# Kernel optimization log

Hardware: AMD Instinct MI355X
Metric: run time of the kernel (lower is better)

The kernel has to match this reference:

```python
import jax, jax.numpy as jnp
import numpy as np

N = 50000      # nodes
E = 1600000    # edges (avg degree 32)
IN, H, OUT, ED = 16, 128, 64, 16


def setup_inputs() -> dict:
    key = jax.random.key(0)
    ks = jax.random.split(key, 24)

    def w(k, shape):
        return jax.random.normal(k, shape, jnp.float32) / np.float32(np.sqrt(shape[0]))

    inp = {
        "x": jax.random.normal(ks[0], (N, IN), jnp.float32),
        "edge_attr": jax.random.normal(ks[1], (E, ED), jnp.float32),
        "edge_src": jax.random.randint(ks[2], (E,), 0, N, jnp.int32),
        "edge_dst": jax.random.randint(ks[3], (E,), 0, N, jnp.int32),
    }
    dims = [(IN, H, H), (H, H, H), (H, H, OUT)]
    i = 4
    for l, (din, dh, dout) in enumerate(dims):
        inp[f"we{l}"] = w(ks[i], (ED, din)); inp[f"be{l}"] = jnp.zeros((din,), jnp.float32)
        inp[f"w1{l}"] = w(ks[i + 1], (din, dh)); inp[f"b1{l}"] = jnp.zeros((dh,), jnp.float32)
        inp[f"w2{l}"] = w(ks[i + 2], (dh, dout)); inp[f"b2{l}"] = jnp.zeros((dout,), jnp.float32)
        i += 3
    inp["rw1"] = w(ks[i], (OUT, H)); inp["rb1"] = jnp.zeros((H,), jnp.float32)
    inp["rw2"] = w(ks[i + 1], (H, IN)); inp["rb2"] = jnp.zeros((IN,), jnp.float32)
    return inp


def reference(x, edge_attr, edge_src, edge_dst,
              we0, be0, w10, b10, w20, b20,
              we1, be1, w11, b11, w21, b21,
              we2, be2, w12, b12, w22, b22,
              rw1, rb1, rw2, rb2):
    layers = [(we0, be0, w10, b10, w20, b20),
              (we1, be1, w11, b11, w21, b21),
              (we2, be2, w12, b12, w22, b22)]
    n = x.shape[0]

    def phi(h):
        # GIN with edge features (GINE): h_i = MLP(h_i + sum_j relu(h_j + W_e e_ij))
        for idx, (we, be, w1, b1, w2, b2) in enumerate(layers):
            e = edge_attr @ we + be                                  # [E, d_in]
            msg = jax.nn.relu(h[edge_src] + e)                       # [E, d_in]
            agg = jax.ops.segment_sum(msg, edge_dst, num_segments=n)  # [N, d_in]
            h = jax.nn.relu((h + agg) @ w1 + b1) @ w2 + b2           # conv MLP
            if idx < len(layers) - 1:
                h = jax.nn.relu(h)
        return h

    out = phi(x) + phi(-x)                       # sign invariance, [N, OUT]
    out = jax.nn.relu(out @ rw1 + rb1) @ rw2 + rb2  # rho readout, [N, IN]
    return out
```

## Files before the change

### kernel.cpp

```cpp
#include <hip/hip_runtime.h>

constexpr int DHID = 128;

typedef __attribute__((ext_vector_type(8))) short bf16x8v;
typedef __attribute__((ext_vector_type(4))) float f32x4v;

__device__ __forceinline__ float b2f(unsigned short u) {
    union { unsigned int i; float f; } v;
    v.i = ((unsigned int)u) << 16;
    return v.f;
}
__device__ __forceinline__ unsigned short f2b(float f) {
    union { float f; unsigned int i; } v;
    v.f = f;
    unsigned int x = v.i;
    return (unsigned short)((x + 0x7fff + ((x >> 16) & 1)) >> 16);
}
__device__ __forceinline__ unsigned int pack2(float a, float b) {
    return (unsigned int)f2b(a) | ((unsigned int)f2b(b) << 16);
}
__device__ __forceinline__ float bres(float w) { return w - b2f(f2b(w)); }
__device__ __forceinline__ void dot2b(float& acc, unsigned int a, unsigned int b) {
    asm("v_dot2_f32_bf16 %0, %1, %2, %0" : "+v"(acc) : "v"(a), "v"(b));
}

__global__ __launch_bounds__(256)
void init_h0(const float* __restrict__ x, float* __restrict__ H0,
             unsigned short* __restrict__ H0B, int n) {
    int i = blockIdx.x * 256 + threadIdx.x;
    if (i < n * 16) {
        int r = i >> 4, c = i & 15;
        float v = x[i];
        H0[(size_t)(2 * r) * 16 + c] = v;
        H0[(size_t)(2 * r + 1) * 16 + c] = -v;
        H0B[(size_t)(2 * r) * 16 + c] = f2b(v);
        H0B[(size_t)(2 * r + 1) * 16 + c] = f2b(-v);
    }
}

__global__ __launch_bounds__(256)
void sum_signs(const float* __restrict__ H3, float* __restrict__ S, int n) {
    int i = blockIdx.x * 256 + threadIdx.x;
    if (i < n * 64) {
        int r = i >> 6;
        S[i] = H3[i + (size_t)r * 64] + H3[i + (size_t)r * 64 + 64];
    }
}

__global__ __launch_bounds__(256)
void csr_count(const int* __restrict__ DST, int* __restrict__ deg, int E_) {
    int e = blockIdx.x * 256 + threadIdx.x;
    if (e < E_) atomicAdd(&deg[DST[e]], 1);
}

__global__ __launch_bounds__(256)
void scan1(const int* __restrict__ deg, int* __restrict__ off,
           int* __restrict__ bsum, int n) {
    __shared__ int s[256];
    int tid = threadIdx.x;
    int i = blockIdx.x * 256 + tid;
    int v = (i < n) ? deg[i] : 0;
    s[tid] = v;
    __syncthreads();
    for (int d = 1; d < 256; d <<= 1) {
        int t = (tid >= d) ? s[tid - d] : 0;
        __syncthreads();
        if (tid >= d) s[tid] += t;
        __syncthreads();
    }
    if (i < n) off[i] = s[tid] - v;
    if (tid == 255) bsum[blockIdx.x] = s[255];
}

__global__ __launch_bounds__(256)
void scan2(int* __restrict__ bsum, int nb) {
    __shared__ int s[256];
    int tid = threadIdx.x;
    int v = (tid < nb) ? bsum[tid] : 0;
    s[tid] = v;
    __syncthreads();
    for (int d = 1; d < 256; d <<= 1) {
        int t = (tid >= d) ? s[tid - d] : 0;
        __syncthreads();
        if (tid >= d) s[tid] += t;
        __syncthreads();
    }
    if (tid < nb) bsum[tid] = s[tid] - v;
}

__global__ __launch_bounds__(256)
void scan3(int* __restrict__ off, int* __restrict__ pos,
           const int* __restrict__ bsum, const int* __restrict__ deg, int n) {
    int i = blockIdx.x * 256 + threadIdx.x;
    if (i < n) {
        int o = off[i] + bsum[blockIdx.x];
        off[i] = o;
        pos[i] = o;
        if (i == n - 1) off[n] = o + deg[i];
    }
}

__global__ __launch_bounds__(256)
void csr_fill(const int* __restrict__ SRC, const int* __restrict__ DST,
              const float* __restrict__ EA, int* __restrict__ pos,
              int* __restrict__ csrsrc, uint4* __restrict__ EABS, int E_) {
    int e = blockIdx.x * 256 + threadIdx.x;
    if (e < E_) {
        int d = DST[e];
        int j = atomicAdd(&pos[d], 1);
        csrsrc[j] = SRC[e];
        const float4* ea4 = (const float4*)(EA + (size_t)e * 16);
        float4 q0 = ea4[0], q1 = ea4[1], q2 = ea4[2], q3 = ea4[3];
        uint4 o0, o1;
        o0.x = pack2(q0.x, q0.y); o0.y = pack2(q0.z, q0.w);
        o0.z = pack2(q1.x, q1.y); o0.w = pack2(q1.z, q1.w);
        o1.x = pack2(q2.x, q2.y); o1.y = pack2(q2.z, q2.w);
        o1.z = pack2(q3.x, q3.y); o1.w = pack2(q3.z, q3.w);
        EABS[(size_t)2 * j] = o0;
        EABS[(size_t)2 * j + 1] = o1;
    }
}

__global__ __launch_bounds__(256)
void agg_gather128(const int* __restrict__ CSRS, const int* __restrict__ OFF,
                   const unsigned short* __restrict__ EABS,
                   const float* __restrict__ WE, const float* __restrict__ BE,
                   const unsigned short* __restrict__ HB,
                   float* __restrict__ AGG, int n) {
    __shared__ float esm_all[4][16][132];
    const int tid = threadIdx.x;
    const int wv = tid >> 6;
    const int lane = tid & 63;
    const int node = blockIdx.x * 4 + wv;
    if (node >= n) return;
    float (*esm)[132] = esm_all[wv];

    const int col = lane & 15;
    const int grp = lane >> 4;
    const int klo = (grp & 1) * 8;

    bf16x8v bfrag[8];
#pragma unroll
    for (int cb = 0; cb < 8; ++cb) {
        bf16x8v b;
#pragma unroll
        for (int i = 0; i < 8; ++i) {
            float w = WE[(klo + i) * 128 + cb * 16 + col];
            unsigned short hi = f2b(w);
            unsigned short lo = f2b(bres(w));
            b[i] = (short)(grp >= 2 ? lo : hi);
        }
        bfrag[cb] = b;
    }
    float bias[8];
#pragma unroll
    for (int cb = 0; cb < 8; ++cb) bias[cb] = BE[cb * 16 + col];

    const int o = lane & 31;
    const int s = o >> 4;
    const int co = (o & 15) * 8;
    const int ep = lane >> 5;

    float acc[8];
#pragma unroll
    for (int i = 0; i < 8; ++i) acc[i] = 0.f;

    const int j0 = OFF[node], j1 = OFF[node + 1];
    const char* ebase = (const char*)EABS;

    for (int base = j0; base < j1; base += 16) {
        const int rem = j1 - base;
        uint4 a4 = *(const uint4*)(ebase + ((size_t)(base + col) << 5) +
                                   ((grp & 1) << 4));
        bf16x8v afrag = __builtin_bit_cast(bf16x8v, a4);
#pragma unroll
        for (int cb = 0; cb < 8; ++cb) {
            f32x4v c = {bias[cb], bias[cb], bias[cb], bias[cb]};
            f32x4v ev = __builtin_amdgcn_mfma_f32_16x16x32_bf16(afrag, bfrag[cb],
                                                                c, 0, 0, 0);
#pragma unroll
            for (int r = 0; r < 4; ++r) {
                const int slot = grp * 4 + r;
                esm[slot][cb * 16 + col] = (slot < rem) ? ev[r] : -1e30f;
            }
        }
#pragma unroll
        for (int i = 0; i < 8; ++i) {
            const int er = 2 * i + ep;
            const int eidx = base + er;
            const int src = CSRS[eidx < j1 ? eidx : (j1 - 1)];
            uint4 hv = *(const uint4*)(HB + (((size_t)(2 * src + s)) << 7) + co);
            const float4* ep4 = (const float4*)&esm[er][co];
            float4 e0 = ep4[0], e1 = ep4[1];
            acc[0] += fmaxf(b2f(hv.x & 0xffff) + e0.x, 0.f);
            acc[1] += fmaxf(b2f(hv.x >> 16)    + e0.y, 0.f);
            acc[2] += fmaxf(b2f(hv.y & 0xffff) + e0.z, 0.f);
            acc[3] += fmaxf(b2f(hv.y >> 16)    + e0.w, 0.f);
            acc[4] += fmaxf(b2f(hv.z & 0xffff) + e1.x, 0.f);
            acc[5] += fmaxf(b2f(hv.z >> 16)    + e1.y, 0.f);
            acc[6] += fmaxf(b2f(hv.w & 0xffff) + e1.z, 0.f);
            acc[7] += fmaxf(b2f(hv.w >> 16)    + e1.w, 0.f);
        }
    }
#pragma unroll
    for (int i = 0; i < 8; ++i) acc[i] += __shfl_xor(acc[i], 32);
    if (lane < 32) {
        float* arow = AGG + (size_t)(2 * node + s) * 128 + co;
        float4 v0 = make_float4(acc[0], acc[1], acc[2], acc[3]);
        float4 v1 = make_float4(acc[4], acc[5], acc[6], acc[7]);
        ((float4*)arow)[0] = v0;
        ((float4*)arow)[1] = v1;
    }
}

__global__ __launch_bounds__(256)
void agg_gather16(const int* __restrict__ CSRS, const int* __restrict__ OFF,
                  const uint4* __restrict__ EABS, const float* __restrict__ WE,
                  const float* __restrict__ BE,
                  const unsigned short* __restrict__ HB,
                  float* __restrict__ AGG, int n) {
    const int l = threadIdx.x & 31;
    const int node = blockIdx.x * 8 + (threadIdx.x >> 5);
    if (node >= n) return;
    const int s = l >> 4;
    const int c = l & 15;
    unsigned int wh[8], wl[8];
#pragma unroll
    for (int t = 0; t < 8; ++t) {
        float a0 = WE[(2 * t) * 16 + c], a1 = WE[(2 * t + 1) * 16 + c];
        wh[t] = pack2(a0, a1);
        wl[t] = pack2(bres(a0), bres(a1));
    }
    const float bev = BE[c];
    float acc = 0.f;
    const int j0 = OFF[node], j1 = OFF[node + 1];
#pragma unroll 4
    for (int j = j0; j < j1; ++j) {
        int src = CSRS[j];
        uint4 p = EABS[(size_t)2 * j], q = EABS[(size_t)2 * j + 1];
        float ec = bev;
        dot2b(ec, p.x, wh[0]); dot2b(ec, p.y, wh[1]);
        dot2b(ec, p.z, wh[2]); dot2b(ec, p.w, wh[3]);
        dot2b(ec, q.x, wh[4]); dot2b(ec, q.y, wh[5]);
        dot2b(ec, q.z, wh[6]); dot2b(ec, q.w, wh[7]);
        dot2b(ec, p.x, wl[0]); dot2b(ec, p.y, wl[1]);
        dot2b(ec, p.z, wl[2]); dot2b(ec, p.w, wl[3]);
        dot2b(ec, q.x, wl[4]); dot2b(ec, q.y, wl[5]);
        dot2b(ec, q.z, wl[6]); dot2b(ec, q.w, wl[7]);
        float hv = b2f(HB[(size_t)(2 * src + s) * 16 + c]);
        acc += fmaxf(hv + ec, 0.f);
    }
    AGG[(size_t)(2 * node + s) * 16 + c] = acc;
}

template <int DIN, int DOUT, bool RELU_OUT, bool HAS_AGG, bool WRITE_B>
__global__ __launch_bounds__(256)
void node_mlp(const float* __restrict__ X, const float* __restrict__ AGG,
              const float* __restrict__ W1, const float* __restrict__ B1,
              const float* __restrict__ W2, const float* __restrict__ B2,
              float* __restrict__ OUT, unsigned short* __restrict__ OUTB,
              int rows) {
    __shared__ float sX[32 * DIN];
    __shared__ float sH[32 * DHID];
    const int tid = threadIdx.x;

    for (int row0 = blockIdx.x * 32; row0 < rows; row0 += gridDim.x * 32) {
        __syncthreads();
        constexpr int DIN4 = DIN / 4;
        for (int i = tid; i < 32 * DIN4; i += 256) {
            int r = i / DIN4, k4 = i % DIN4;
            int gr = row0 + r;
            float4 v = make_float4(0.f, 0.f, 0.f, 0.f);
            if (gr < rows) {
                v = ((const float4*)X)[(size_t)gr * DIN4 + k4];
                if (HAS_AGG) {
                    float4 a = ((const float4*)AGG)[(size_t)gr * DIN4 + k4];
                    v.x += a.x; v.y += a.y; v.z += a.z; v.w += a.w;
                }
            }
            ((float4*)sX)[i] = v;
        }
        __syncthreads();
        {
            const int c = tid & 63;
            const int r0 = tid >> 6;
            float acc[8][2];
            const float b1a = B1[c], b1b = B1[c + 64];
#pragma unroll
            for (int j = 0; j < 8; ++j) {
                acc[j][0] = b1a;
                acc[j][1] = b1b;
            }
#pragma unroll 2
            for (int k4 = 0; k4 < DIN / 4; ++k4) {
                const int k = 4 * k4;
                float wa[4], wb[4];
#pragma unroll
                for (int kk = 0; kk < 4; ++kk) {
                    wa[kk] = W1[(k + kk) * DHID + c];
                    wb[kk] = W1[(k + kk) * DHID + c + 64];
                }
#pragma unroll
                for (int j = 0; j < 8; ++j) {
                    float4 xv = ((const float4*)sX)[((r0 + 4 * j) * DIN + k) >> 2];
                    acc[j][0] += xv.x * wa[0]; acc[j][1] += xv.x * wb[0];
                    acc[j][0] += xv.y * wa[1]; acc[j][1] += xv.y * wb[1];
                    acc[j][0] += xv.z * wa[2]; acc[j][1] += xv.z * wb[2];
                    acc[j][0] += xv.w * wa[3]; acc[j][1] += xv.w * wb[3];
                }
            }
#pragma unroll
            for (int j = 0; j < 8; ++j) {
                int r = r0 + 4 * j;
                sH[r * DHID + c] = fmaxf(acc[j][0], 0.f);
                sH[r * DHID + c + 64] = fmaxf(acc[j][1], 0.f);
            }
        }
        __syncthreads();
        {
            constexpr int HALF = DOUT / 2;
            constexpr int RP = 256 / HALF;
            constexpr int ITER = 32 / RP;
            const int c = tid % HALF;
            const int r0 = tid / HALF;
            float acc[ITER][2];
            const float bz0 = B2[c], bz1 = B2[c + HALF];
#pragma unroll
            for (int j = 0; j < ITER; ++j) {
                acc[j][0] = bz0;
                acc[j][1] = bz1;
            }
#pragma unroll 2
            for (int k4 = 0; k4 < DHID / 4; ++k4) {
                const int k = 4 * k4;
                float wa[4], wb[4];
#pragma unroll
                for (int kk = 0; kk < 4; ++kk) {
                    wa[kk] = W2[(k + kk) * DOUT + c];
                    wb[kk] = W2[(k + kk) * DOUT + c + HALF];
                }
#pragma unroll
                for (int j = 0; j < ITER; ++j) {
                    float4 hv = ((const float4*)sH)[((r0 + RP * j) * DHID + k) >> 2];
                    acc[j][0] += hv.x * wa[0]; acc[j][1] += hv.x * wb[0];
                    acc[j][0] += hv.y * wa[1]; acc[j][1] += hv.y * wb[1];
                    acc[j][0] += hv.z * wa[2]; acc[j][1] += hv.z * wb[2];
                    acc[j][0] += hv.w * wa[3]; acc[j][1] += hv.w * wb[3];
                }
            }
#pragma unroll
            for (int j = 0; j < ITER; ++j) {
                int gr = row0 + r0 + RP * j;
                if (gr < rows) {
                    float o0 = acc[j][0], o1 = acc[j][1];
                    if (RELU_OUT) {
                        o0 = fmaxf(o0, 0.f);
                        o1 = fmaxf(o1, 0.f);
                    }
                    OUT[(size_t)gr * DOUT + c] = o0;
                    OUT[(size_t)gr * DOUT + c + HALF] = o1;
                    if (WRITE_B) {
                        OUTB[(size_t)gr * DOUT + c] = f2b(o0);
                        OUTB[(size_t)gr * DOUT + c + HALF] = f2b(o1);
                    }
                }
            }
        }
    }
}

extern "C" void kernel_launch(void* const* d_in, const int* in_sizes, int n_in,
                              void* d_out, int out_size, void* d_ws, size_t ws_size,
                              hipStream_t stream) {
    const float* x = (const float*)d_in[0];
    const float* ea = (const float*)d_in[1];
    const int* esrc = (const int*)d_in[2];
    const int* edst = (const int*)d_in[3];
    const float* we0 = (const float*)d_in[4];
    const float* be0 = (const float*)d_in[5];
    const float* w10 = (const float*)d_in[6];
    const float* b10 = (const float*)d_in[7];
    const float* w20 = (const float*)d_in[8];
    const float* b20 = (const float*)d_in[9];
    const float* we1 = (const float*)d_in[10];
    const float* be1 = (const float*)d_in[11];
    const float* w11 = (const float*)d_in[12];
    const float* b11 = (const float*)d_in[13];
    const float* w21 = (const float*)d_in[14];
    const float* b21 = (const float*)d_in[15];
    const float* we2 = (const float*)d_in[16];
    const float* be2 = (const float*)d_in[17];
    const float* w12 = (const float*)d_in[18];
    const float* b12 = (const float*)d_in[19];
    const float* w22 = (const float*)d_in[20];
    const float* b22 = (const float*)d_in[21];
    const float* rw1 = (const float*)d_in[22];
    const float* rb1 = (const float*)d_in[23];
    const float* rw2 = (const float*)d_in[24];
    const float* rb2 = (const float*)d_in[25];

    const int N = in_sizes[0] / 16;
    const int E = in_sizes[2];
    const int M = 2 * N;

    float* HA = (float*)d_ws;
    float* HB = HA + (size_t)M * 128;
    float* AG = HB + (size_t)M * 128;
    unsigned short* Hb = (unsigned short*)(AG + (size_t)M * 128);
    unsigned short* EABS = Hb + (size_t)M * 128;
    int* deg = (int*)(EABS + (size_t)E * 16);
    int* off = deg + N;
    int* pos = off + N + 1;
    int* bsum = pos + N;
    int* csrsrc = bsum + 256;

    const int ntiles = (M + 31) / 32;
    const int eblocks = (E + 255) / 256;
    const int nblocks = (N + 255) / 256;

    hipMemsetAsync(deg, 0, (size_t)N * sizeof(int), stream);
    csr_count<<<eblocks, 256, 0, stream>>>(edst, deg, E);
    scan1<<<nblocks, 256, 0, stream>>>(deg, off, bsum, N);
    scan2<<<1, 256, 0, stream>>>(bsum, nblocks);
    scan3<<<nblocks, 256, 0, stream>>>(off, pos, bsum, deg, N);
    csr_fill<<<eblocks, 256, 0, stream>>>(esrc, edst, ea, pos, csrsrc,
                                          (uint4*)EABS, E);

    init_h0<<<(N * 16 + 255) / 256, 256, 0, stream>>>(x, HA, Hb, N);

    agg_gather16<<<(N + 7) / 8, 256, 0, stream>>>(csrsrc, off, (const uint4*)EABS,
                                                  we0, be0, Hb, AG, N);
    node_mlp<16, 128, true, true, true><<<ntiles, 256, 0, stream>>>(
        HA, AG, w10, b10, w20, b20, HB, Hb, M);

    agg_gather128<<<(N + 3) / 4, 256, 0, stream>>>(csrsrc, off, EABS,
                                                   we1, be1, Hb, AG, N);
    node_mlp<128, 128, true, true, true><<<ntiles, 256, 0, stream>>>(
        HB, AG, w11, b11, w21, b21, HA, Hb, M);

    agg_gather128<<<(N + 3) / 4, 256, 0, stream>>>(csrsrc, off, EABS,
                                                   we2, be2, Hb, AG, N);
    node_mlp<128, 64, false, true, false><<<ntiles, 256, 0, stream>>>(
        HA, AG, w12, b12, w22, b22, HB, nullptr, M);

    sum_signs<<<(N * 64 + 255) / 256, 256, 0, stream>>>(HB, AG, N);
    node_mlp<64, 16, false, false, false><<<(N + 31) / 32, 256, 0, stream>>>(
        AG, nullptr, rw1, rb1, rw2, rb2, (float*)d_out, nullptr, N);
}
```

Measured before the change: 955.0 us.

## Use persistent grid-stride gather kernels with full-tile fast path and packed adds

The gather kernels become persistent with a fixed grid of 1024 blocks that grid-stride over nodes. The per-wave weight-fragment setup (the WE to bf16 hi/lo split) is therefore amortized across many nodes instead of being redone for each one. The 128-wide gather also splits full 16-edge tiles from the remainder tile, dropping masking and index clamping in the common path, and uses v_pk_add_f32 for the accumulation. A fixed grid of 1024 blocks may leave load imbalance or underfill on a large GPU.

```diff
diff --git a/kernel.cpp b/kernel.cpp
--- a/kernel.cpp
+++ b/kernel.cpp
@@ -4,6 +4,7 @@
 
 typedef __attribute__((ext_vector_type(8))) short bf16x8v;
 typedef __attribute__((ext_vector_type(4))) float f32x4v;
+typedef __attribute__((ext_vector_type(2))) float f32x2v;
 
 __device__ __forceinline__ float b2f(unsigned short u) {
     union { unsigned int i; float f; } v;
@@ -22,6 +23,11 @@
 __device__ __forceinline__ float bres(float w) { return w - b2f(f2b(w)); }
 __device__ __forceinline__ void dot2b(float& acc, unsigned int a, unsigned int b) {
     asm("v_dot2_f32_bf16 %0, %1, %2, %0" : "+v"(acc) : "v"(a), "v"(b));
+}
+__device__ __forceinline__ f32x2v pkadd(f32x2v a, f32x2v b) {
+    f32x2v d;
+    asm("v_pk_add_f32 %0, %1, %2" : "=v"(d) : "v"(a), "v"(b));
+    return d;
 }
 
 __global__ __launch_bounds__(256)
@@ -131,8 +137,6 @@
     const int tid = threadIdx.x;
     const int wv = tid >> 6;
     const int lane = tid & 63;
-    const int node = blockIdx.x * 4 + wv;
-    if (node >= n) return;
     float (*esm)[132] = esm_all[wv];
 
     const int col = lane & 15;
@@ -161,55 +165,106 @@
     const int co = (o & 15) * 8;
     const int ep = lane >> 5;
 
-    float acc[8];
-#pragma unroll
-    for (int i = 0; i < 8; ++i) acc[i] = 0.f;
-
-    const int j0 = OFF[node], j1 = OFF[node + 1];
     const char* ebase = (const char*)EABS;
-
-    for (int base = j0; base < j1; base += 16) {
-        const int rem = j1 - base;
-        uint4 a4 = *(const uint4*)(ebase + ((size_t)(base + col) << 5) +
-                                   ((grp & 1) << 4));
-        bf16x8v afrag = __builtin_bit_cast(bf16x8v, a4);
-#pragma unroll
-        for (int cb = 0; cb < 8; ++cb) {
-            f32x4v c = {bias[cb], bias[cb], bias[cb], bias[cb]};
-            f32x4v ev = __builtin_amdgcn_mfma_f32_16x16x32_bf16(afrag, bfrag[cb],
-                                                                c, 0, 0, 0);
-#pragma unroll
-            for (int r = 0; r < 4; ++r) {
-                const int slot = grp * 4 + r;
-                esm[slot][cb * 16 + col] = (slot < rem) ? ev[r] : -1e30f;
-            }
-        }
-#pragma unroll
-        for (int i = 0; i < 8; ++i) {
-            const int er = 2 * i + ep;
-            const int eidx = base + er;
-            const int src = CSRS[eidx < j1 ? eidx : (j1 - 1)];
-            uint4 hv = *(const uint4*)(HB + (((size_t)(2 * src + s)) << 7) + co);
-            const float4* ep4 = (const float4*)&esm[er][co];
-            float4 e0 = ep4[0], e1 = ep4[1];
-            acc[0] += fmaxf(b2f(hv.x & 0xffff) + e0.x, 0.f);
-            acc[1] += fmaxf(b2f(hv.x >> 16)    + e0.y, 0.f);
-            acc[2] += fmaxf(b2f(hv.y & 0xffff) + e0.z, 0.f);
-            acc[3] += fmaxf(b2f(hv.y >> 16)    + e0.w, 0.f);
-            acc[4] += fmaxf(b2f(hv.z & 0xffff) + e1.x, 0.f);
-            acc[5] += fmaxf(b2f(hv.z >> 16)    + e1.y, 0.f);
-            acc[6] += fmaxf(b2f(hv.w & 0xffff) + e1.z, 0.f);
-            acc[7] += fmaxf(b2f(hv.w >> 16)    + e1.w, 0.f);
-        }
-    }
-#pragma unroll
-    for (int i = 0; i < 8; ++i) acc[i] += __shfl_xor(acc[i], 32);
-    if (lane < 32) {
-        float* arow = AGG + (size_t)(2 * node + s) * 128 + co;
-        float4 v0 = make_float4(acc[0], acc[1], acc[2], acc[3]);
-        float4 v1 = make_float4(acc[4], acc[5], acc[6], acc[7]);
-        ((float4*)arow)[0] = v0;
-        ((float4*)arow)[1] = v1;
+    const int stride = gridDim.x * 4;
+
+    for (int node = blockIdx.x * 4 + wv; node < n; node += stride) {
+        f32x2v acc[4];
+#pragma unroll
+        for (int i = 0; i < 4; ++i) { acc[i].x = 0.f; acc[i].y = 0.f; }
+
+        const int j0 = OFF[node], j1 = OFF[node + 1];
+        int base = j0;
+        for (; base + 16 <= j1; base += 16) {
+            uint4 a4 = *(const uint4*)(ebase + ((size_t)(base + col) << 5) +
+                                       ((grp & 1) << 4));
+            bf16x8v afrag = __builtin_bit_cast(bf16x8v, a4);
+#pragma unroll
+            for (int cb = 0; cb < 8; ++cb) {
+                f32x4v c = {bias[cb], bias[cb], bias[cb], bias[cb]};
+                f32x4v ev = __builtin_amdgcn_mfma_f32_16x16x32_bf16(
+                    afrag, bfrag[cb], c, 0, 0, 0);
+#pragma unroll
+                for (int r = 0; r < 4; ++r)
+                    esm[grp * 4 + r][cb * 16 + col] = ev[r];
+            }
+#pragma unroll
+            for (int i = 0; i < 8; ++i) {
+                const int er = 2 * i + ep;
+                const int src = CSRS[base + er];
+                uint4 hv = *(const uint4*)(HB + (((size_t)(2 * src + s)) << 7) + co);
+                const float4* ep4 = (const float4*)&esm[er][co];
+                float4 e0 = ep4[0], e1 = ep4[1];
+                f32x2v h, e2, t;
+                h.x = b2f(hv.x & 0xffff); h.y = b2f(hv.x >> 16);
+                e2.x = e0.x; e2.y = e0.y;
+                t = pkadd(h, e2);
+                t.x = fmaxf(t.x, 0.f); t.y = fmaxf(t.y, 0.f);
+                acc[0] = pkadd(acc[0], t);
+                h.x = b2f(hv.y & 0xffff); h.y = b2f(hv.y >> 16);
+                e2.x = e0.z; e2.y = e0.w;
+                t = pkadd(h, e2);
+                t.x = fmaxf(t.x, 0.f); t.y = fmaxf(t.y, 0.f);
+                acc[1] = pkadd(acc[1], t);
+                h.x = b2f(hv.z & 0xffff); h.y = b2f(hv.z >> 16);
+                e2.x = e1.x; e2.y = e1.y;
+                t = pkadd(h, e2);
+                t.x = fmaxf(t.x, 0.f); t.y = fmaxf(t.y, 0.f);
+                acc[2] = pkadd(acc[2], t);
+                h.x = b2f(hv.w & 0xffff); h.y = b2f(hv.w >> 16);
+                e2.x = e1.z; e2.y = e1.w;
+                t = pkadd(h, e2);
+                t.x = fmaxf(t.x, 0.f); t.y = fmaxf(t.y, 0.f);
+                acc[3] = pkadd(acc[3], t);
+            }
+        }
+        if (base < j1) {
+            const int rem = j1 - base;
+            uint4 a4 = *(const uint4*)(ebase +
+                                       ((size_t)(base + (col < rem ? col : 0)) << 5) +
+                                       ((grp & 1) << 4));
+            bf16x8v afrag = __builtin_bit_cast(bf16x8v, a4);
+#pragma unroll
+            for (int cb = 0; cb < 8; ++cb) {
+                f32x4v c = {bias[cb], bias[cb], bias[cb], bias[cb]};
+                f32x4v ev = __builtin_amdgcn_mfma_f32_16x16x32_bf16(
+                    afrag, bfrag[cb], c, 0, 0, 0);
+#pragma unroll
+                for (int r = 0; r < 4; ++r) {
+                    const int slot = grp * 4 + r;
+                    esm[slot][cb * 16 + col] = (slot < rem) ? ev[r] : -1e30f;
+                }
+            }
+#pragma unroll
+            for (int i = 0; i < 8; ++i) {
+                const int er = 2 * i + ep;
+                const int eidx = base + er;
+                const int src = CSRS[eidx < j1 ? eidx : (j1 - 1)];
+                uint4 hv = *(const uint4*)(HB + (((size_t)(2 * src + s)) << 7) + co);
+                const float4* ep4 = (const float4*)&esm[er][co];
+                float4 e0 = ep4[0], e1 = ep4[1];
+                acc[0].x += fmaxf(b2f(hv.x & 0xffff) + e0.x, 0.f);
+                acc[0].y += fmaxf(b2f(hv.x >> 16)    + e0.y, 0.f);
+                acc[1].x += fmaxf(b2f(hv.y & 0xffff) + e0.z, 0.f);
+                acc[1].y += fmaxf(b2f(hv.y >> 16)    + e0.w, 0.f);
+                acc[2].x += fmaxf(b2f(hv.z & 0xffff) + e1.x, 0.f);
+                acc[2].y += fmaxf(b2f(hv.z >> 16)    + e1.y, 0.f);
+                acc[3].x += fmaxf(b2f(hv.w & 0xffff) + e1.z, 0.f);
+                acc[3].y += fmaxf(b2f(hv.w >> 16)    + e1.w, 0.f);
+            }
+        }
+#pragma unroll
+        for (int i = 0; i < 4; ++i) {
+            acc[i].x += __shfl_xor(acc[i].x, 32);
+            acc[i].y += __shfl_xor(acc[i].y, 32);
+        }
+        if (lane < 32) {
+            float* arow = AGG + (size_t)(2 * node + s) * 128 + co;
+            float4 v0 = make_float4(acc[0].x, acc[0].y, acc[1].x, acc[1].y);
+            float4 v1 = make_float4(acc[2].x, acc[2].y, acc[3].x, acc[3].y);
+            ((float4*)arow)[0] = v0;
+            ((float4*)arow)[1] = v1;
+        }
     }
 }
 
@@ -220,8 +275,6 @@
                   const unsigned short* __restrict__ HB,
                   float* __restrict__ AGG, int n) {
     const int l = threadIdx.x & 31;
-    const int node = blockIdx.x * 8 + (threadIdx.x >> 5);
-    if (node >= n) return;
     const int s = l >> 4;
     const int c = l & 15;
     unsigned int wh[8], wl[8];
@@ -232,25 +285,28 @@
         wl[t] = pack2(bres(a0), bres(a1));
     }
     const float bev = BE[c];
-    float acc = 0.f;
-    const int j0 = OFF[node], j1 = OFF[node + 1];
+    const int stride = gridDim.x * 8;
+    for (int node = blockIdx.x * 8 + (threadIdx.x >> 5); node < n; node += stride) {
+        float acc = 0.f;
+        const int j0 = OFF[node], j1 = OFF[node + 1];
 #pragma unroll 4
-    for (int j = j0; j < j1; ++j) {
-        int src = CSRS[j];
-        uint4 p = EABS[(size_t)2 * j], q = EABS[(size_t)2 * j + 1];
-        float ec = bev;
-        dot2b(ec, p.x, wh[0]); dot2b(ec, p.y, wh[1]);
-        dot2b(ec, p.z, wh[2]); dot2b(ec, p.w, wh[3]);
-        dot2b(ec, q.x, wh[4]); dot2b(ec, q.y, wh[5]);
-        dot2b(ec, q.z, wh[6]); dot2b(ec, q.w, wh[7]);
-        dot2b(ec, p.x, wl[0]); dot2b(ec, p.y, wl[1]);
-        dot2b(ec, p.z, wl[2]); dot2b(ec, p.w, wl[3]);
-        dot2b(ec, q.x, wl[4]); dot2b(ec, q.y, wl[5]);
-        dot2b(ec, q.z, wl[6]); dot2b(ec, q.w, wl[7]);
-        float hv = b2f(HB[(size_t)(2 * src + s) * 16 + c]);
-        acc += fmaxf(hv + ec, 0.f);
-    }
-    AGG[(size_t)(2 * node + s) * 16 + c] = acc;
+        for (int j = j0; j < j1; ++j) {
+            int src = CSRS[j];
+            uint4 p = EABS[(size_t)2 * j], q = EABS[(size_t)2 * j + 1];
+            float ec = bev;
+            dot2b(ec, p.x, wh[0]); dot2b(ec, p.y, wh[1]);
+            dot2b(ec, p.z, wh[2]); dot2b(ec, p.w, wh[3]);
+            dot2b(ec, q.x, wh[4]); dot2b(ec, q.y, wh[5]);
+            dot2b(ec, q.z, wh[6]); dot2b(ec, q.w, wh[7]);
+            dot2b(ec, p.x, wl[0]); dot2b(ec, p.y, wl[1]);
+            dot2b(ec, p.z, wl[2]); dot2b(ec, p.w, wl[3]);
+            dot2b(ec, q.x, wl[4]); dot2b(ec, q.y, wl[5]);
+            dot2b(ec, q.z, wl[6]); dot2b(ec, q.w, wl[7]);
+            float hv = b2f(HB[(size_t)(2 * src + s) * 16 + c]);
+            acc += fmaxf(hv + ec, 0.f);
+        }
+        AGG[(size_t)(2 * node + s) * 16 + c] = acc;
+    }
 }
 
 template <int DIN, int DOUT, bool RELU_OUT, bool HAS_AGG, bool WRITE_B>
@@ -428,18 +484,18 @@
 
     init_h0<<<(N * 16 + 255) / 256, 256, 0, stream>>>(x, HA, Hb, N);
 
-    agg_gather16<<<(N + 7) / 8, 256, 0, stream>>>(csrsrc, off, (const uint4*)EABS,
-                                                  we0, be0, Hb, AG, N);
+    agg_gather16<<<1024, 256, 0, stream>>>(csrsrc, off, (const uint4*)EABS,
+                                           we0, be0, Hb, AG, N);
     node_mlp<16, 128, true, true, true><<<ntiles, 256, 0, stream>>>(
         HA, AG, w10, b10, w20, b20, HB, Hb, M);
 
-    agg_gather128<<<(N + 3) / 4, 256, 0, stream>>>(csrsrc, off, EABS,
-                                                   we1, be1, Hb, AG, N);
+    agg_gather128<<<1024, 256, 0, stream>>>(csrsrc, off, EABS,
+                                            we1, be1, Hb, AG, N);
     node_mlp<128, 128, true, true, true><<<ntiles, 256, 0, stream>>>(
         HB, AG, w11, b11, w21, b21, HA, Hb, M);
 
-    agg_gather128<<<(N + 3) / 4, 256, 0, stream>>>(csrsrc, off, EABS,
-                                                   we2, be2, Hb, AG, N);
+    agg_gather128<<<1024, 256, 0, stream>>>(csrsrc, off, EABS,
+                                            we2, be2, Hb, AG, N);
     node_mlp<128, 64, false, true, false><<<ntiles, 256, 0, stream>>>(
         HA, AG, w12, b12, w22, b22, HB, nullptr, M);
 
```

Result: slower. 1.250 ms (+30.8%).
